# Kernel optimization log

Hardware: AMD Instinct MI355X
Metric: run time of the kernel (lower is better)

Reference implementation:

```python
import jax, jax.numpy as jnp
import numpy as np

GROUP_SIZE = 16
E2M1_MAX = 6.0
# Positive E2M1 grid and midpoints for round-to-nearest
E2M1_POS = jnp.array([0.0, 0.5, 1.0, 1.5, 2.0, 3.0, 4.0, 6.0], jnp.float32)
E2M1_MID = jnp.array([0.25, 0.75, 1.25, 1.75, 2.5, 3.5, 5.0], jnp.float32)
# Full 16-entry signed LUT (bit3 = sign, sign-magnitude)
E2M1_LUT = jnp.array([0.0, 0.5, 1.0, 1.5, 2.0, 3.0, 4.0, 6.0,
                      -0.0, -0.5, -1.0, -1.5, -2.0, -3.0, -4.0, -6.0], jnp.float32)

def _round_e2m1(x):
    # nearest value on the E2M1 grid (clamped to +-6)
    idx = jnp.searchsorted(E2M1_MID, jnp.abs(x))
    return jnp.sign(x) * E2M1_POS[idx]

def nvfp4_act_qdq(x, input_scale):
    # per-group dynamic quantize to NVFP4 with fp8-e4m3 group scale, then dequantize
    orig_shape = x.shape
    xg = x.astype(jnp.float32).reshape(*orig_shape[:-1], -1, GROUP_SIZE)
    amax = jnp.max(jnp.abs(xg), axis=-1, keepdims=True)
    s = (amax / (E2M1_MAX * input_scale)).astype(jnp.float8_e4m3fn).astype(jnp.float32)
    s = jnp.where(s > 0, s, 1.0)
    total = s * input_scale  # effective per-group scale
    dq = _round_e2m1(xg / total) * total
    return dq.reshape(orig_shape).astype(jnp.float16)

def nvfp4_dequantize(weight, weight_scale, weight_scale_2):
    # weight: [O, I//2] packed bytes (values 0..255); low nibble = even index
    O = weight.shape[0]
    low = weight & 0xF
    high = (weight >> 4) & 0xF
    codes = jnp.stack([low, high], axis=-1).reshape(O, -1)  # [O, I]
    vals = E2M1_LUT[codes].reshape(O, -1, GROUP_SIZE)       # [O, G, 16]
    w = vals * weight_scale[:, :, None] * weight_scale_2
    return w.reshape(O, -1).astype(jnp.float16)

def setup_inputs() -> dict:
    key = jax.random.key(0)
    k1, k2, k3 = jax.random.split(key, 3)
    B, S, I, O = 8, 16, 8192, 8192
    hidden_states = jax.random.normal(k1, (B, S, I), dtype=jnp.float16)
    weight = jax.random.randint(k2, (O, I // 2), 0, 256, dtype=jnp.int32)
    weight_scale = jax.random.uniform(k3, (O, I // GROUP_SIZE), dtype=jnp.float32) * 0.05 + 0.001
    weight_scale_2 = jnp.ones((1,), jnp.float32)
    input_scale = jnp.ones((1,), jnp.float32)
    return {"hidden_states": hidden_states, "weight": weight,
            "weight_scale": weight_scale, "weight_scale_2": weight_scale_2,
            "input_scale": input_scale}

def reference(hidden_states, weight, weight_scale, weight_scale_2, input_scale):
    hs_dq = nvfp4_act_qdq(hidden_states, input_scale)
    w_dq = nvfp4_dequantize(weight, weight_scale, weight_scale_2)
    return jnp.matmul(hs_dq, w_dq.T)  # [B, S, O], fp16
```

## Files before the change

kernel.cpp:

```cpp
#include <hip/hip_runtime.h>
#include <stdint.h>


typedef _Float16 half8 __attribute__((ext_vector_type(8)));
typedef float float4v __attribute__((ext_vector_type(4)));

__device__ __forceinline__ uint32_t perm_b32(uint32_t hi, uint32_t lo, uint32_t sel) {
  return __builtin_amdgcn_perm(hi, lo, sel);
}

__device__ __forceinline__ void load_lds16(const uint4* g, uint4* l) {
  __builtin_amdgcn_global_load_lds((const __attribute__((address_space(1))) void*)g,
                                   (__attribute__((address_space(3))) void*)l,
                                   16, 0, 0);
}

__device__ __forceinline__ float e4m3_roundtrip(float x) {
  if (x < 0.015625f) {
    return __builtin_rintf(x * 512.0f) * 0.001953125f;
  }
  uint32_t u = __float_as_uint(x);
  u += 0x7FFFFu + ((u >> 20) & 1u);
  u &= 0xFFF00000u;
  float y = __uint_as_float(u);
  return fminf(y, 448.0f);
}

__global__ __launch_bounds__(256)
void aqdq_kernel(const float* __restrict__ hs,
                 const float* __restrict__ isc,
                 uint2* __restrict__ asw) {
  const int t = blockIdx.x * 256 + threadIdx.x;
  const int m = t >> 11;
  const int u = t & 2047;
  const int g = u >> 2;
  const int hq = u & 3;

  const float* p = hs + m * 8192 + g * 16 + hq * 4;
  float4 x = *(const float4*)p;

  float amax = fmaxf(fmaxf(fabsf(x.x), fabsf(x.y)), fmaxf(fabsf(x.z), fabsf(x.w)));
  amax = fmaxf(amax, __shfl_xor(amax, 1));
  amax = fmaxf(amax, __shfl_xor(amax, 2));

  float is = isc[0];
  float s = e4m3_roundtrip(amax / (6.0f * is));
  if (!(s > 0.0f)) s = 1.0f;
  float total = s * is;

  float xv[4] = {x.x, x.y, x.z, x.w};
  union { _Float16 h[4]; uint2 v; } qq;
#pragma unroll
  for (int i = 0; i < 4; ++i) {
    float r = xv[i] / total;
    float a = fabsf(r);
    float v = (a <= 0.25f) ? 0.0f
            : (a <= 0.75f) ? 0.5f
            : (a <= 1.25f) ? 1.0f
            : (a <= 1.75f) ? 1.5f
            : (a <= 2.5f)  ? 2.0f
            : (a <= 3.5f)  ? 3.0f
            : (a <= 5.0f)  ? 4.0f : 6.0f;
    qq.h[i] = (_Float16)(copysignf(v, r) * total);
  }

  const int k = g * 16 + hq * 4;
  const int kb = k >> 5;
  const int quad = (k >> 3) & 3;
  const int lane16 = (m & 15) | (quad << 4);
  const int mb = m >> 4;
  asw[((kb * 8 + mb) * 64 + lane16) * 2 + (hq & 1)] = qq.v;
}

__device__ __forceinline__ half8 decode_scale(int4 w, float sf) {
  uint32_t t0 = perm_b32((uint32_t)w.y, (uint32_t)w.x, 0x00000400u);
  uint32_t t1 = perm_b32((uint32_t)w.w, (uint32_t)w.z, 0x04000000u);
  uint32_t b  = perm_b32(t1, t0, 0x07060100u);
  uint32_t ev = b & 0x0F0F0F0Fu;
  uint32_t od = (b >> 4) & 0x0F0F0F0Fu;
  uint32_t evm = ev & 0x07070707u;
  uint32_t odm = od & 0x07070707u;
  uint32_t evs = (ev & 0x08080808u) << 4;
  uint32_t ods = (od & 0x08080808u) << 4;
  uint32_t evh = perm_b32(0x46444240u, 0x3E3C3800u, evm) | evs;
  uint32_t odh = perm_b32(0x46444240u, 0x3E3C3800u, odm) | ods;
  union { uint32_t u[4]; half8 h; } r;
  r.u[0] = perm_b32(odh, evh, 0x04000000u) & 0xFF00FF00u;
  r.u[1] = perm_b32(odh, evh, 0x05000100u) & 0xFF00FF00u;
  r.u[2] = perm_b32(odh, evh, 0x06000200u) & 0xFF00FF00u;
  r.u[3] = perm_b32(odh, evh, 0x07000300u) & 0xFF00FF00u;
  _Float16 hsf = (_Float16)sf;
  half8 sv = {hsf, hsf, hsf, hsf, hsf, hsf, hsf, hsf};
  return r.h * sv;
}

template<int MODE>
__global__ __launch_bounds__(512, 4)
void gemm_kernel(const uint4* __restrict__ asw,
                 const int* __restrict__ wq,
                 const float* __restrict__ wsc,
                 const float* __restrict__ ws2p,
                 float* __restrict__ dst) {
  __shared__ uint4 abuf[4][8][64];
  const int lane = threadIdx.x & 63;
  const int wv = threadIdx.x >> 6;
  const int quad = lane >> 4;
  const int kp = blockIdx.x & 7;
  const int nb = blockIdx.x >> 3;
  const int col = nb * 128 + wv * 16 + (lane & 15);
  const float ws2 = ws2p[0];
  const int4* wp = (const int4*)(wq + (size_t)col * 4096) + kp * 128 + quad;
  const float2* sp = (const float2*)(wsc + (size_t)col * 512 + kp * 64);
  const uint4* ap = asw + kp * 16384 + wv * 64 + lane;

  float4v acc[8];
#pragma unroll
  for (int mb = 0; mb < 8; ++mb) acc[mb] = (float4v){0.f, 0.f, 0.f, 0.f};

  int4 wreg[4];
  float2 sreg[4];

  load_lds16(ap, &abuf[0][wv][0]);
  wreg[0] = wp[0];
  sreg[0] = sp[0];
  load_lds16(ap + 512, &abuf[1][wv][0]);
  wreg[1] = wp[4];
  sreg[1] = sp[1];

#define STEP_BODY(J, STAGE_EN, VMCNT_N)                                           \
  {                                                                               \
    if (STAGE_EN) {                                                               \
      load_lds16(apg + ((J) + 2) * 512, &abuf[((J) + 2) & 3][wv][0]);             \
      wreg[((J) + 2) & 3] = wpg[((J) + 2) * 4];                                   \
      sreg[((J) + 2) & 3] = spg[(J) + 2];                                         \
    }                                                                             \
    __builtin_amdgcn_sched_barrier(0);                                            \
    asm volatile("s_waitcnt vmcnt(" #VMCNT_N ")" ::: "memory");                   \
    __builtin_amdgcn_s_barrier();                                                 \
    __builtin_amdgcn_sched_barrier(0);                                            \
    uint4 af[8];                                                                  \
    _Pragma("unroll")                                                             \
    for (int mb = 0; mb < 8; ++mb) af[mb] = abuf[(J)][mb][lane];                  \
    float sA = ((quad & 2) ? sreg[(J)].y : sreg[(J)].x) * ws2;                    \
    half8 bA = decode_scale(wreg[(J)], sA);                                       \
    _Pragma("unroll")                                                             \
    for (int mb = 0; mb < 8; ++mb) {                                              \
      union { uint4 u; half8 h; } a;                                              \
      a.u = af[mb];                                                               \
      acc[mb] = __builtin_amdgcn_mfma_f32_16x16x32_f16(a.h, bA, acc[mb], 0, 0, 0);\
    }                                                                             \
  }

  {
    const uint4* apg = ap;
    const int4* wpg = wp;
    const float2* spg = sp;
    for (int tt = 0; tt < 28; tt += 4) {
      STEP_BODY(0, true, 6)
      STEP_BODY(1, true, 6)
      STEP_BODY(2, true, 6)
      STEP_BODY(3, true, 6)
      apg += 4 * 512;
      wpg += 16;
      spg += 4;
    }
    STEP_BODY(0, true, 6)
    STEP_BODY(1, true, 6)
    STEP_BODY(2, false, 3)
    STEP_BODY(3, false, 0)
  }
#undef STEP_BODY

  if (MODE == 0) {
    float* pp = dst + ((size_t)kp << 20) + col;
#pragma unroll
    for (int mb = 0; mb < 8; ++mb) {
      const int mrow = mb * 16 + quad * 4;
#pragma unroll
      for (int r = 0; r < 4; ++r) pp[(size_t)(mrow + r) * 8192] = acc[mb][r];
    }
  } else {
#pragma unroll
    for (int mb = 0; mb < 8; ++mb) {
      const int mrow = mb * 16 + quad * 4;
#pragma unroll
      for (int r = 0; r < 4; ++r)
        unsafeAtomicAdd(&dst[(size_t)(mrow + r) * 8192 + col], acc[mb][r]);
    }
  }
}

__global__ __launch_bounds__(256)
void reduce_kernel(const float4* __restrict__ part, float4* __restrict__ out) {
  const int i = blockIdx.x * 256 + threadIdx.x;
  float4 s = part[i];
#pragma unroll
  for (int p = 1; p < 8; ++p) {
    float4 b = part[(size_t)p * 262144 + i];
    s.x += b.x; s.y += b.y; s.z += b.z; s.w += b.w;
  }
  out[i] = s;
}

extern "C" void kernel_launch(void* const* d_in, const int* in_sizes, int n_in,
                              void* d_out, int out_size, void* d_ws, size_t ws_size,
                              hipStream_t stream) {
  (void)in_sizes; (void)n_in; (void)out_size;
  const float* hs  = (const float*)d_in[0];
  const int* wq    = (const int*)d_in[1];
  const float* wsc = (const float*)d_in[2];
  const float* ws2 = (const float*)d_in[3];
  const float* isc = (const float*)d_in[4];
  float* out       = (float*)d_out;
  uint2* asw2      = (uint2*)d_ws;
  const uint4* asw4 = (const uint4*)d_ws;

  aqdq_kernel<<<1024, 256, 0, stream>>>(hs, isc, asw2);

  const size_t need = ((size_t)2 << 20) + ((size_t)32 << 20);
  if (ws_size >= need) {
    float* part = (float*)((char*)d_ws + ((size_t)2 << 20));
    gemm_kernel<0><<<512, 512, 0, stream>>>(asw4, wq, wsc, ws2, part);
    reduce_kernel<<<1024, 256, 0, stream>>>((const float4*)part, (float4*)out);
  } else {
    hipMemsetAsync(out, 0, (size_t)128 * 8192 * 4, stream);
    gemm_kernel<1><<<512, 512, 0, stream>>>(asw4, wq, wsc, ws2, out);
  }
}
```

Baseline: 243.9 us.

## Stage packed weights through swizzled LDS with coalesced bulk loads

Instead of each lane fetching its own 16-byte weight chunk per k-step with strided row access, each wave loads 16 full weight rows for its k-slice in coalesced 16-byte chunks up front. It pre-packs the low bytes and writes them into a double-buffered, XOR-swizzled LDS tile, and each step reads one 32-bit word back for decoding. The aim is better global-memory coalescing for the weight stream. In exchange it adds 64 KB of shared memory, 16 int4 staging registers per thread, and lowers the launch-bounds occupancy hint from 4 to 2.

```diff
diff --git a/kernel.cpp b/kernel.cpp
--- a/kernel.cpp
+++ b/kernel.cpp
@@ -72,10 +72,7 @@
   asw[((kb * 8 + mb) * 64 + lane16) * 2 + (hq & 1)] = qq.v;
 }
 
-__device__ __forceinline__ half8 decode_scale(int4 w, float sf) {
-  uint32_t t0 = perm_b32((uint32_t)w.y, (uint32_t)w.x, 0x00000400u);
-  uint32_t t1 = perm_b32((uint32_t)w.w, (uint32_t)w.z, 0x04000000u);
-  uint32_t b  = perm_b32(t1, t0, 0x07060100u);
+__device__ __forceinline__ half8 decode_u32(uint32_t b, float sf) {
   uint32_t ev = b & 0x0F0F0F0Fu;
   uint32_t od = (b >> 4) & 0x0F0F0F0Fu;
   uint32_t evm = ev & 0x07070707u;
@@ -95,13 +92,14 @@
 }
 
 template<int MODE>
-__global__ __launch_bounds__(512, 4)
+__global__ __launch_bounds__(512, 2)
 void gemm_kernel(const uint4* __restrict__ asw,
                  const int* __restrict__ wq,
                  const float* __restrict__ wsc,
                  const float* __restrict__ ws2p,
                  float* __restrict__ dst) {
   __shared__ uint4 abuf[4][8][64];
+  __shared__ uint32_t wtile[2][8192];
   const int lane = threadIdx.x & 63;
   const int wv = threadIdx.x >> 6;
   const int quad = lane >> 4;
@@ -109,67 +107,113 @@
   const int nb = blockIdx.x >> 3;
   const int col = nb * 128 + wv * 16 + (lane & 15);
   const float ws2 = ws2p[0];
-  const int4* wp = (const int4*)(wq + (size_t)col * 4096) + kp * 128 + quad;
   const float2* sp = (const float2*)(wsc + (size_t)col * 512 + kp * 64);
   const uint4* ap = asw + kp * 16384 + wv * 64 + lane;
+  const int4* wbase = (const int4*)wq;
+  const int scol0 = nb * 128 + wv * 16;
+  const int ws_s = lane >> 2;
+  const int ws_q = lane & 3;
 
   float4v acc[8];
 #pragma unroll
   for (int mb = 0; mb < 8; ++mb) acc[mb] = (float4v){0.f, 0.f, 0.f, 0.f};
 
-  int4 wreg[4];
   float2 sreg[4];
-
+  int4 wst[16];
+
+#pragma unroll
+  for (int j = 0; j < 16; ++j)
+    wst[j] = wbase[(scol0 + j) * 1024 + kp * 128 + lane];
   load_lds16(ap, &abuf[0][wv][0]);
-  wreg[0] = wp[0];
   sreg[0] = sp[0];
   load_lds16(ap + 512, &abuf[1][wv][0]);
-  wreg[1] = wp[4];
   sreg[1] = sp[1];
-
-#define STEP_BODY(J, STAGE_EN, VMCNT_N)                                           \
+  __builtin_amdgcn_sched_barrier(0);
+  asm volatile("s_waitcnt vmcnt(4)" ::: "memory");
+  __builtin_amdgcn_sched_barrier(0);
+#pragma unroll
+  for (int j = 0; j < 16; ++j) {
+    int4 w = wst[j];
+    uint32_t p0 = perm_b32((uint32_t)w.y, (uint32_t)w.x, 0x00000400u);
+    uint32_t p1 = perm_b32((uint32_t)w.w, (uint32_t)w.z, 0x00000400u);
+    uint32_t b  = perm_b32(p1, p0, 0x05040100u);
+    const int cl = wv * 16 + j;
+    wtile[0][ws_s * 512 + (((cl * 4 + ws_q) ^ ((ws_s & 7) << 2)))] = b;
+  }
+#pragma unroll
+  for (int j = 0; j < 16; ++j)
+    wst[j] = wbase[(scol0 + j) * 1024 + kp * 128 + 64 + lane];
+
+#define STEP(T, VN, STG, X1)                                                      \
   {                                                                               \
-    if (STAGE_EN) {                                                               \
-      load_lds16(apg + ((J) + 2) * 512, &abuf[((J) + 2) & 3][wv][0]);             \
-      wreg[((J) + 2) & 3] = wpg[((J) + 2) * 4];                                   \
-      sreg[((J) + 2) & 3] = spg[(J) + 2];                                         \
+    if (STG) {                                                                    \
+      load_lds16(ap + ((T) + 2) * 512, &abuf[((T) + 2) & 3][wv][0]);              \
+      sreg[((T) + 2) & 3] = sp[(T) + 2];                                          \
     }                                                                             \
     __builtin_amdgcn_sched_barrier(0);                                            \
-    asm volatile("s_waitcnt vmcnt(" #VMCNT_N ")" ::: "memory");                   \
+    asm volatile("s_waitcnt vmcnt(" #VN ")" ::: "memory");                        \
     __builtin_amdgcn_s_barrier();                                                 \
     __builtin_amdgcn_sched_barrier(0);                                            \
     uint4 af[8];                                                                  \
     _Pragma("unroll")                                                             \
-    for (int mb = 0; mb < 8; ++mb) af[mb] = abuf[(J)][mb][lane];                  \
-    float sA = ((quad & 2) ? sreg[(J)].y : sreg[(J)].x) * ws2;                    \
-    half8 bA = decode_scale(wreg[(J)], sA);                                       \
+    for (int mb = 0; mb < 8; ++mb) af[mb] = abuf[(T) & 3][mb][lane];              \
+    const int s_ = (T) & 15;                                                      \
+    uint32_t wb_ = wtile[((T) >> 4) & 1]                                          \
+        [s_ * 512 + ((((wv * 16 + (lane & 15)) * 4 + quad)) ^ ((s_ & 7) << 2))];  \
+    float sA = ((quad & 2) ? sreg[(T) & 3].y : sreg[(T) & 3].x) * ws2;            \
+    half8 bA = decode_u32(wb_, sA);                                               \
     _Pragma("unroll")                                                             \
     for (int mb = 0; mb < 8; ++mb) {                                              \
-      union { uint4 u; half8 h; } a;                                              \
-      a.u = af[mb];                                                               \
-      acc[mb] = __builtin_amdgcn_mfma_f32_16x16x32_f16(a.h, bA, acc[mb], 0, 0, 0);\
+      union { uint4 u; half8 h; } a_;                                             \
+      a_.u = af[mb];                                                              \
+      acc[mb] = __builtin_amdgcn_mfma_f32_16x16x32_f16(a_.h, bA, acc[mb], 0, 0, 0);\
     }                                                                             \
-  }
-
-  {
-    const uint4* apg = ap;
-    const int4* wpg = wp;
-    const float2* spg = sp;
-    for (int tt = 0; tt < 28; tt += 4) {
-      STEP_BODY(0, true, 6)
-      STEP_BODY(1, true, 6)
-      STEP_BODY(2, true, 6)
-      STEP_BODY(3, true, 6)
-      apg += 4 * 512;
-      wpg += 16;
-      spg += 4;
-    }
-    STEP_BODY(0, true, 6)
-    STEP_BODY(1, true, 6)
-    STEP_BODY(2, false, 3)
-    STEP_BODY(3, false, 0)
-  }
-#undef STEP_BODY
+    if (X1) {                                                                     \
+      _Pragma("unroll")                                                           \
+      for (int j = 0; j < 16; ++j) {                                              \
+        int4 w = wst[j];                                                          \
+        uint32_t p0 = perm_b32((uint32_t)w.y, (uint32_t)w.x, 0x00000400u);        \
+        uint32_t p1 = perm_b32((uint32_t)w.w, (uint32_t)w.z, 0x00000400u);        \
+        uint32_t b  = perm_b32(p1, p0, 0x05040100u);                              \
+        const int cl = wv * 16 + j;                                               \
+        wtile[1][ws_s * 512 + (((cl * 4 + ws_q) ^ ((ws_s & 7) << 2)))] = b;       \
+      }                                                                           \
+    }                                                                             \
+  }
+
+  STEP(0, 20, 1, 0)
+  STEP(1, 20, 1, 0)
+  STEP(2, 4, 1, 1)
+  STEP(3, 4, 1, 0)
+  STEP(4, 4, 1, 0)
+  STEP(5, 4, 1, 0)
+  STEP(6, 4, 1, 0)
+  STEP(7, 4, 1, 0)
+  STEP(8, 4, 1, 0)
+  STEP(9, 4, 1, 0)
+  STEP(10, 4, 1, 0)
+  STEP(11, 4, 1, 0)
+  STEP(12, 4, 1, 0)
+  STEP(13, 4, 1, 0)
+  STEP(14, 4, 1, 0)
+  STEP(15, 4, 1, 0)
+  STEP(16, 4, 1, 0)
+  STEP(17, 4, 1, 0)
+  STEP(18, 4, 1, 0)
+  STEP(19, 4, 1, 0)
+  STEP(20, 4, 1, 0)
+  STEP(21, 4, 1, 0)
+  STEP(22, 4, 1, 0)
+  STEP(23, 4, 1, 0)
+  STEP(24, 4, 1, 0)
+  STEP(25, 4, 1, 0)
+  STEP(26, 4, 1, 0)
+  STEP(27, 4, 1, 0)
+  STEP(28, 4, 1, 0)
+  STEP(29, 4, 1, 0)
+  STEP(30, 2, 0, 0)
+  STEP(31, 0, 0, 0)
+#undef STEP
 
   if (MODE == 0) {
     float* pp = dst + ((size_t)kp << 20) + col;
```

Measured after the change: 241.5 us. Within noise of the previous version (-1.0%).

## Stage packed weights through swizzled LDS tile with coalesced int2 loads

Applied to the files above, without the earlier changes.

Replaces the per-lane strided int4 weight loads with coalesced int2 loads across 8 columns per wave. Each lane keeps only the low byte of every int32 element, packs two bytes, and writes them into a double-buffered, XOR-swizzled 32KB LDS tile. The MFMA steps then read one uint32 per lane from LDS and decode it. The weight prefetch is interleaved by hand with the A-tile pipeline using explicit vmcnt waits. This aims to cut wasted bandwidth and uncoalesced access on the int32-stored weights, at the cost of extra LDS capacity (possible occupancy loss), more registers, and a fragile hand-tuned wait schedule.

```diff
diff --git a/kernel.cpp b/kernel.cpp
--- a/kernel.cpp
+++ b/kernel.cpp
@@ -72,10 +72,7 @@
   asw[((kb * 8 + mb) * 64 + lane16) * 2 + (hq & 1)] = qq.v;
 }
 
-__device__ __forceinline__ half8 decode_scale(int4 w, float sf) {
-  uint32_t t0 = perm_b32((uint32_t)w.y, (uint32_t)w.x, 0x00000400u);
-  uint32_t t1 = perm_b32((uint32_t)w.w, (uint32_t)w.z, 0x04000000u);
-  uint32_t b  = perm_b32(t1, t0, 0x07060100u);
+__device__ __forceinline__ half8 decode_u32(uint32_t b, float sf) {
   uint32_t ev = b & 0x0F0F0F0Fu;
   uint32_t od = (b >> 4) & 0x0F0F0F0Fu;
   uint32_t evm = ev & 0x07070707u;
@@ -102,6 +99,8 @@
                  const float* __restrict__ ws2p,
                  float* __restrict__ dst) {
   __shared__ uint4 abuf[4][8][64];
+  __shared__ uint32_t wtile32[8192];
+  uint16_t* wtile16 = (uint16_t*)wtile32;
   const int lane = threadIdx.x & 63;
   const int wv = threadIdx.x >> 6;
   const int quad = lane >> 4;
@@ -109,67 +108,128 @@
   const int nb = blockIdx.x >> 3;
   const int col = nb * 128 + wv * 16 + (lane & 15);
   const float ws2 = ws2p[0];
-  const int4* wp = (const int4*)(wq + (size_t)col * 4096) + kp * 128 + quad;
   const float2* sp = (const float2*)(wsc + (size_t)col * 512 + kp * 64);
   const uint4* ap = asw + kp * 16384 + wv * 64 + lane;
+  const int2* wp2 = (const int2*)wq;
+  const int scol0 = nb * 128 + wv * 16;
 
   float4v acc[8];
 #pragma unroll
   for (int mb = 0; mb < 8; ++mb) acc[mb] = (float4v){0.f, 0.f, 0.f, 0.f};
 
-  int4 wreg[4];
   float2 sreg[4];
-
+  int2 wsta[8], wstb[8];
+
+#define W_ISSUE(DST, QQ, HALF)                                                    \
+  {                                                                               \
+    _Pragma("unroll")                                                             \
+    for (int j = 0; j < 8; ++j)                                                   \
+      DST[j] = wp2[(size_t)(scol0 + (HALF) * 8 + j) * 2048 + kp * 256 +           \
+                   (QQ) * 64 + lane];                                             \
+    __builtin_amdgcn_sched_barrier(0);                                            \
+  }
+
+#define W_EXTRACT(SRC, QQ, HALF)                                                  \
+  {                                                                               \
+    __builtin_amdgcn_sched_barrier(0);                                            \
+    const int s_loc = lane >> 3;                                                  \
+    const int qd = (lane >> 1) & 3;                                               \
+    const int hh = lane & 1;                                                      \
+    _Pragma("unroll")                                                             \
+    for (int j = 0; j < 8; ++j) {                                                 \
+      uint32_t v = perm_b32((uint32_t)SRC[j].y, (uint32_t)SRC[j].x, 0x0C0C0400u); \
+      const int cl = wv * 16 + (HALF) * 8 + j;                                    \
+      wtile16[((((QQ) & 1) * 4096) + s_loc * 512 +                                \
+               ((cl * 4 + qd) ^ (s_loc << 2))) * 2 + hh] = (uint16_t)v;           \
+    }                                                                             \
+    asm volatile("s_waitcnt lgkmcnt(0)" ::: "memory");                            \
+    __builtin_amdgcn_sched_barrier(0);                                            \
+  }
+
+#define STEP(T, VN)                                                               \
+  {                                                                               \
+    if ((T) < 30) {                                                               \
+      load_lds16(ap + ((T) + 2) * 512, &abuf[((T) + 2) & 3][wv][0]);              \
+      sreg[((T) + 2) & 3] = sp[(T) + 2];                                          \
+    }                                                                             \
+    __builtin_amdgcn_sched_barrier(0);                                            \
+    asm volatile("s_waitcnt vmcnt(" #VN ")" ::: "memory");                        \
+    __builtin_amdgcn_s_barrier();                                                 \
+    __builtin_amdgcn_sched_barrier(0);                                            \
+    uint4 af[8];                                                                  \
+    _Pragma("unroll")                                                             \
+    for (int mb = 0; mb < 8; ++mb) af[mb] = abuf[(T) & 3][mb][lane];              \
+    const int s_ = (T) & 7;                                                       \
+    uint32_t wb_ = wtile32[(((T) >> 3) & 1) * 4096 + s_ * 512 +                   \
+                           (((wv * 16 + (lane & 15)) * 4 + quad) ^ (s_ << 2))];   \
+    float sA = ((quad & 2) ? sreg[(T) & 3].y : sreg[(T) & 3].x) * ws2;            \
+    half8 bA = decode_u32(wb_, sA);                                               \
+    _Pragma("unroll")                                                             \
+    for (int mb = 0; mb < 8; ++mb) {                                              \
+      union { uint4 u; half8 h; } a_;                                             \
+      a_.u = af[mb];                                                              \
+      acc[mb] = __builtin_amdgcn_mfma_f32_16x16x32_f16(a_.h, bA, acc[mb], 0, 0, 0);\
+    }                                                                             \
+  }
+
+  W_ISSUE(wsta, 0, 0)
+  W_ISSUE(wstb, 0, 1)
   load_lds16(ap, &abuf[0][wv][0]);
-  wreg[0] = wp[0];
   sreg[0] = sp[0];
   load_lds16(ap + 512, &abuf[1][wv][0]);
-  wreg[1] = wp[4];
   sreg[1] = sp[1];
-
-#define STEP_BODY(J, STAGE_EN, VMCNT_N)                                           \
-  {                                                                               \
-    if (STAGE_EN) {                                                               \
-      load_lds16(apg + ((J) + 2) * 512, &abuf[((J) + 2) & 3][wv][0]);             \
-      wreg[((J) + 2) & 3] = wpg[((J) + 2) * 4];                                   \
-      sreg[((J) + 2) & 3] = spg[(J) + 2];                                         \
-    }                                                                             \
-    __builtin_amdgcn_sched_barrier(0);                                            \
-    asm volatile("s_waitcnt vmcnt(" #VMCNT_N ")" ::: "memory");                   \
-    __builtin_amdgcn_s_barrier();                                                 \
-    __builtin_amdgcn_sched_barrier(0);                                            \
-    uint4 af[8];                                                                  \
-    _Pragma("unroll")                                                             \
-    for (int mb = 0; mb < 8; ++mb) af[mb] = abuf[(J)][mb][lane];                  \
-    float sA = ((quad & 2) ? sreg[(J)].y : sreg[(J)].x) * ws2;                    \
-    half8 bA = decode_scale(wreg[(J)], sA);                                       \
-    _Pragma("unroll")                                                             \
-    for (int mb = 0; mb < 8; ++mb) {                                              \
-      union { uint4 u; half8 h; } a;                                              \
-      a.u = af[mb];                                                               \
-      acc[mb] = __builtin_amdgcn_mfma_f32_16x16x32_f16(a.h, bA, acc[mb], 0, 0, 0);\
-    }                                                                             \
-  }
-
-  {
-    const uint4* apg = ap;
-    const int4* wpg = wp;
-    const float2* spg = sp;
-    for (int tt = 0; tt < 28; tt += 4) {
-      STEP_BODY(0, true, 6)
-      STEP_BODY(1, true, 6)
-      STEP_BODY(2, true, 6)
-      STEP_BODY(3, true, 6)
-      apg += 4 * 512;
-      wpg += 16;
-      spg += 4;
-    }
-    STEP_BODY(0, true, 6)
-    STEP_BODY(1, true, 6)
-    STEP_BODY(2, false, 3)
-    STEP_BODY(3, false, 0)
-  }
-#undef STEP_BODY
+  __builtin_amdgcn_sched_barrier(0);
+  asm volatile("s_waitcnt vmcnt(4)" ::: "memory");
+  W_EXTRACT(wsta, 0, 0)
+  W_EXTRACT(wstb, 0, 1)
+  W_ISSUE(wsta, 1, 0)
+  W_ISSUE(wstb, 1, 1)
+
+  STEP(0, 20)
+  STEP(1, 20)
+  STEP(2, 4)
+  W_EXTRACT(wsta, 1, 0)
+  W_EXTRACT(wstb, 1, 1)
+  STEP(3, 4)
+  STEP(4, 4)
+  STEP(5, 4)
+  W_ISSUE(wsta, 2, 0)
+  STEP(6, 12)
+  W_ISSUE(wstb, 2, 1)
+  STEP(7, 20)
+  STEP(8, 12)
+  W_EXTRACT(wsta, 2, 0)
+  STEP(9, 4)
+  W_EXTRACT(wstb, 2, 1)
+  STEP(10, 4)
+  STEP(11, 4)
+  STEP(12, 4)
+  STEP(13, 4)
+  W_ISSUE(wsta, 3, 0)
+  STEP(14, 12)
+  W_ISSUE(wstb, 3, 1)
+  STEP(15, 20)
+  STEP(16, 12)
+  W_EXTRACT(wsta, 3, 0)
+  STEP(17, 4)
+  W_EXTRACT(wstb, 3, 1)
+  STEP(18, 4)
+  STEP(19, 4)
+  STEP(20, 4)
+  STEP(21, 4)
+  STEP(22, 4)
+  STEP(23, 4)
+  STEP(24, 4)
+  STEP(25, 4)
+  STEP(26, 4)
+  STEP(27, 4)
+  STEP(28, 4)
+  STEP(29, 4)
+  STEP(30, 2)
+  STEP(31, 0)
+#undef STEP
+#undef W_ISSUE
+#undef W_EXTRACT
 
   if (MODE == 0) {
     float* pp = dst + ((size_t)kp << 20) + col;
```

After: 269.6 us. 1.11x slower.

## Stage weight tiles through swizzled LDS with coalesced loads and finer split-K

Applied to the files above, without the earlier changes.

The GEMM now uses 256-thread blocks covering 64 columns and splits K 16 ways instead of 8. Each wave preloads its whole weight slab (packed 4-bit codes) and scales into XOR-swizzled LDS using contiguous per-row loads, instead of strided per-lane int4 loads during the K loop. Activations are double-buffered in LDS. This makes weight reads coalesced, but doubles the partial-sum buffer and the reduce traffic.

```diff
diff --git a/kernel.cpp b/kernel.cpp
--- a/kernel.cpp
+++ b/kernel.cpp
@@ -13,6 +13,12 @@
   __builtin_amdgcn_global_load_lds((const __attribute__((address_space(1))) void*)g,
                                    (__attribute__((address_space(3))) void*)l,
                                    16, 0, 0);
+}
+
+__device__ __forceinline__ uint32_t pack4(int4 w) {
+  uint32_t t0 = perm_b32((uint32_t)w.y, (uint32_t)w.x, 0x00000400u);
+  uint32_t t1 = perm_b32((uint32_t)w.w, (uint32_t)w.z, 0x04000000u);
+  return perm_b32(t1, t0, 0x07060100u);
 }
 
 __device__ __forceinline__ float e4m3_roundtrip(float x) {
@@ -72,10 +78,7 @@
   asw[((kb * 8 + mb) * 64 + lane16) * 2 + (hq & 1)] = qq.v;
 }
 
-__device__ __forceinline__ half8 decode_scale(int4 w, float sf) {
-  uint32_t t0 = perm_b32((uint32_t)w.y, (uint32_t)w.x, 0x00000400u);
-  uint32_t t1 = perm_b32((uint32_t)w.w, (uint32_t)w.z, 0x04000000u);
-  uint32_t b  = perm_b32(t1, t0, 0x07060100u);
+__device__ __forceinline__ half8 decode_u32(uint32_t b, float sf) {
   uint32_t ev = b & 0x0F0F0F0Fu;
   uint32_t od = (b >> 4) & 0x0F0F0F0Fu;
   uint32_t evm = ev & 0x07070707u;
@@ -95,84 +98,109 @@
 }
 
 template<int MODE>
-__global__ __launch_bounds__(512, 4)
+__global__ __launch_bounds__(256, 4)
 void gemm_kernel(const uint4* __restrict__ asw,
                  const int* __restrict__ wq,
                  const float* __restrict__ wsc,
                  const float* __restrict__ ws2p,
                  float* __restrict__ dst) {
-  __shared__ uint4 abuf[4][8][64];
+  __shared__ uint4 abuf[2][8][64];
+  __shared__ uint32_t wlds[4096];
+  __shared__ float slds[2048];
   const int lane = threadIdx.x & 63;
   const int wv = threadIdx.x >> 6;
   const int quad = lane >> 4;
-  const int kp = blockIdx.x & 7;
-  const int nb = blockIdx.x >> 3;
-  const int col = nb * 128 + wv * 16 + (lane & 15);
+  const int ks = blockIdx.x & 15;
+  const int nb = blockIdx.x >> 4;
+  const int colg0 = nb * 64 + wv * 16;
+  const int col = colg0 + (lane & 15);
   const float ws2 = ws2p[0];
-  const int4* wp = (const int4*)(wq + (size_t)col * 4096) + kp * 128 + quad;
-  const float2* sp = (const float2*)(wsc + (size_t)col * 512 + kp * 64);
-  const uint4* ap = asw + kp * 16384 + wv * 64 + lane;
+  const int4* wr = (const int4*)wq;
+  const uint4* apA = asw + ((size_t)(ks * 16) * 8 + wv * 2) * 64 + lane;
+  const uint4* apB = apA + 64;
+  const int sW = lane >> 2;
+  const int qW = lane & 3;
 
   float4v acc[8];
 #pragma unroll
   for (int mb = 0; mb < 8; ++mb) acc[mb] = (float4v){0.f, 0.f, 0.f, 0.f};
 
-  int4 wreg[4];
-  float2 sreg[4];
-
-  load_lds16(ap, &abuf[0][wv][0]);
-  wreg[0] = wp[0];
-  sreg[0] = sp[0];
-  load_lds16(ap + 512, &abuf[1][wv][0]);
-  wreg[1] = wp[4];
-  sreg[1] = sp[1];
-
-#define STEP_BODY(J, STAGE_EN, VMCNT_N)                                           \
+  load_lds16(apA, &abuf[0][wv * 2][0]);
+  load_lds16(apB, &abuf[0][wv * 2 + 1][0]);
+
+  int4 wr0, wr1, wr2, wr3, wr4, wr5, wr6, wr7;
+#define W_ISSUE4(R0, R1, R2, R3, CB)                                              \
+  R0 = wr[(size_t)(colg0 + (CB) + 0) * 1024 + ks * 64 + lane];                    \
+  R1 = wr[(size_t)(colg0 + (CB) + 1) * 1024 + ks * 64 + lane];                    \
+  R2 = wr[(size_t)(colg0 + (CB) + 2) * 1024 + ks * 64 + lane];                    \
+  R3 = wr[(size_t)(colg0 + (CB) + 3) * 1024 + ks * 64 + lane];                    \
+  __builtin_amdgcn_sched_barrier(0);
+
+#define W_WRITE4(R0, R1, R2, R3, CB)                                              \
   {                                                                               \
-    if (STAGE_EN) {                                                               \
-      load_lds16(apg + ((J) + 2) * 512, &abuf[((J) + 2) & 3][wv][0]);             \
-      wreg[((J) + 2) & 3] = wpg[((J) + 2) * 4];                                   \
-      sreg[((J) + 2) & 3] = spg[(J) + 2];                                         \
+    uint32_t b0 = pack4(R0), b1 = pack4(R1), b2 = pack4(R2), b3 = pack4(R3);      \
+    wlds[wv * 1024 + ((CB) + 0) * 64 + ((sW ^ (((CB) + 0) & 7)) << 2) + qW] = b0; \
+    wlds[wv * 1024 + ((CB) + 1) * 64 + ((sW ^ (((CB) + 1) & 7)) << 2) + qW] = b1; \
+    wlds[wv * 1024 + ((CB) + 2) * 64 + ((sW ^ (((CB) + 2) & 7)) << 2) + qW] = b2; \
+    wlds[wv * 1024 + ((CB) + 3) * 64 + ((sW ^ (((CB) + 3) & 7)) << 2) + qW] = b3; \
+    __builtin_amdgcn_sched_barrier(0);                                            \
+  }
+
+  W_ISSUE4(wr0, wr1, wr2, wr3, 0)
+  W_ISSUE4(wr4, wr5, wr6, wr7, 4)
+  W_WRITE4(wr0, wr1, wr2, wr3, 0)
+  W_ISSUE4(wr0, wr1, wr2, wr3, 8)
+  W_WRITE4(wr4, wr5, wr6, wr7, 4)
+  W_ISSUE4(wr4, wr5, wr6, wr7, 12)
+  W_WRITE4(wr0, wr1, wr2, wr3, 8)
+  {
+    const float* sb = wsc + (size_t)(colg0 + (lane >> 2)) * 512 + ks * 32 + (lane & 3) * 8;
+    float4v s0 = *(const float4v*)sb;
+    float4v s1 = *(const float4v*)(sb + 4);
+    W_WRITE4(wr4, wr5, wr6, wr7, 12)
+    const int cS = lane >> 2;
+    const int G0 = (lane & 3) * 2;
+    *(float4v*)&slds[wv * 512 + cS * 32 + ((G0 ^ (cS & 7)) << 2)] = s0;
+    *(float4v*)&slds[wv * 512 + cS * 32 + (((G0 | 1) ^ (cS & 7)) << 2)] = s1;
+  }
+#undef W_ISSUE4
+#undef W_WRITE4
+
+#define STEP(T)                                                                   \
+  {                                                                               \
+    __syncthreads();    \
+                        \
+    __builtin_amdgcn_sched_barrier(0);                                            \
+    if ((T) < 15) {                                                               \
+      load_lds16(apA + ((T) + 1) * 512, &abuf[((T) + 1) & 1][wv * 2][0]);         \
+      load_lds16(apB + ((T) + 1) * 512, &abuf[((T) + 1) & 1][wv * 2 + 1][0]);     \
     }                                                                             \
-    __builtin_amdgcn_sched_barrier(0);                                            \
-    asm volatile("s_waitcnt vmcnt(" #VMCNT_N ")" ::: "memory");                   \
-    __builtin_amdgcn_s_barrier();                                                 \
     __builtin_amdgcn_sched_barrier(0);                                            \
     uint4 af[8];                                                                  \
     _Pragma("unroll")                                                             \
-    for (int mb = 0; mb < 8; ++mb) af[mb] = abuf[(J)][mb][lane];                  \
-    float sA = ((quad & 2) ? sreg[(J)].y : sreg[(J)].x) * ws2;                    \
-    half8 bA = decode_scale(wreg[(J)], sA);                                       \
+    for (int mb = 0; mb < 8; ++mb) af[mb] = abuf[(T) & 1][mb][lane];              \
+    uint32_t wb = wlds[wv * 1024 + (lane & 15) * 64 +                             \
+                       (((T) ^ (lane & 7)) << 2) + (lane >> 4)];                  \
+    const int g_ = 2 * (T) + (quad >> 1);                                         \
+    float sc = slds[wv * 512 + (lane & 15) * 32 +                                 \
+                    (((g_ >> 2) ^ (lane & 7)) << 2) + (g_ & 3)] * ws2;            \
+    half8 bA = decode_u32(wb, sc);                                                \
     _Pragma("unroll")                                                             \
     for (int mb = 0; mb < 8; ++mb) {                                              \
-      union { uint4 u; half8 h; } a;                                              \
-      a.u = af[mb];                                                               \
-      acc[mb] = __builtin_amdgcn_mfma_f32_16x16x32_f16(a.h, bA, acc[mb], 0, 0, 0);\
+      union { uint4 u; half8 h; } a_;                                             \
+      a_.u = af[mb];                                                              \
+      acc[mb] = __builtin_amdgcn_mfma_f32_16x16x32_f16(a_.h, bA, acc[mb], 0, 0, 0);\
     }                                                                             \
   }
 
-  {
-    const uint4* apg = ap;
-    const int4* wpg = wp;
-    const float2* spg = sp;
-    for (int tt = 0; tt < 28; tt += 4) {
-      STEP_BODY(0, true, 6)
-      STEP_BODY(1, true, 6)
-      STEP_BODY(2, true, 6)
-      STEP_BODY(3, true, 6)
-      apg += 4 * 512;
-      wpg += 16;
-      spg += 4;
-    }
-    STEP_BODY(0, true, 6)
-    STEP_BODY(1, true, 6)
-    STEP_BODY(2, false, 3)
-    STEP_BODY(3, false, 0)
-  }
-#undef STEP_BODY
+  STEP(0)  STEP(1)  STEP(2)  STEP(3)
+  STEP(4)  STEP(5)  STEP(6)  STEP(7)
+  STEP(8)  STEP(9)  STEP(10) STEP(11)
+  STEP(12) STEP(13) STEP(14) STEP(15)
+#undef STEP
 
   if (MODE == 0) {
-    float* pp = dst + ((size_t)kp << 20) + col;
+    float* pp = dst + ((size_t)ks << 20) + col;
 #pragma unroll
     for (int mb = 0; mb < 8; ++mb) {
       const int mrow = mb * 16 + quad * 4;
@@ -195,7 +223,7 @@
   const int i = blockIdx.x * 256 + threadIdx.x;
   float4 s = part[i];
 #pragma unroll
-  for (int p = 1; p < 8; ++p) {
+  for (int p = 1; p < 16; ++p) {
     float4 b = part[(size_t)p * 262144 + i];
     s.x += b.x; s.y += b.y; s.z += b.z; s.w += b.w;
   }
@@ -217,13 +245,13 @@
 
   aqdq_kernel<<<1024, 256, 0, stream>>>(hs, isc, asw2);
 
-  const size_t need = ((size_t)2 << 20) + ((size_t)32 << 20);
+  const size_t need = ((size_t)2 << 20) + ((size_t)64 << 20);
   if (ws_size >= need) {
     float* part = (float*)((char*)d_ws + ((size_t)2 << 20));
-    gemm_kernel<0><<<512, 512, 0, stream>>>(asw4, wq, wsc, ws2, part);
+    gemm_kernel<0><<<2048, 256, 0, stream>>>(asw4, wq, wsc, ws2, part);
     reduce_kernel<<<1024, 256, 0, stream>>>((const float4*)part, (float4*)out);
   } else {
     hipMemsetAsync(out, 0, (size_t)128 * 8192 * 4, stream);
-    gemm_kernel<1><<<512, 512, 0, stream>>>(asw4, wq, wsc, ws2, out);
-  }
-}
+    gemm_kernel<1><<<2048, 256, 0, stream>>>(asw4, wq, wsc, ws2, out);
+  }
+}
```

New measurement: 248.5 us. No clear change (+1.9%).
